# Kernel optimization log

Hardware: AMD Instinct MI355X
Metric: run time of the kernel (lower is better)

The kernel has to match this reference:

```python
import jax, jax.numpy as jnp
from jax import lax
import numpy as np

B = 4096
L = 20  # nb_latents


def conv2d(x, w, b, stride, pad):
    y = lax.conv_general_dilated(x, w, (stride, stride), [(pad, pad), (pad, pad)],
                                 dimension_numbers=('NCHW', 'OIHW', 'NCHW'))
    return y + b[None, :, None, None]


def deconv2d(x, w, b, stride, pad):
    # w has PyTorch ConvTranspose2d layout [Cin, Cout, kh, kw]
    k = w.shape[2]
    w2 = jnp.flip(w, (2, 3)).transpose(1, 0, 2, 3)  # -> [Cout, Cin, kh, kw]
    y = lax.conv_general_dilated(x, w2, (1, 1), [(k - 1 - pad,) * 2] * 2,
                                 lhs_dilation=(stride, stride),
                                 dimension_numbers=('NCHW', 'OIHW', 'NCHW'))
    return y + b[None, :, None, None]


def setup_inputs() -> dict:
    key = jax.random.key(0)
    ks = jax.random.split(key, 16)

    def W(k, shape, fan_in, scale=1.0):
        return (jax.random.normal(k, shape, jnp.float32) * (scale / np.sqrt(fan_in))).astype(jnp.float32)

    z = lambda n: jnp.zeros((n,), jnp.float32)
    return {
        'x': jax.random.uniform(ks[0], (B, 1, 28, 28), jnp.float32),
        'eps': jax.random.normal(ks[1], (B, L), jnp.float32),
        'w_c1': W(ks[2], (32, 1, 4, 4), 16), 'b_c1': z(32),
        'w_c2': W(ks[3], (32, 32, 4, 4), 512), 'b_c2': z(32),
        'w_c3': W(ks[4], (64, 32, 3, 3), 288), 'b_c3': z(64),
        'w_fc1': W(ks[5], (256, 1024), 1024), 'b_fc1': z(256),
        'w_mu': W(ks[6], (L, 256), 256), 'b_mu': z(L),
        # small scale + negative bias keeps the 100-step exp(logvar) recursion in fp32 range
        'w_ls': W(ks[7], (L, 256), 256, 0.1), 'b_ls': jnp.full((L,), -2.0, jnp.float32),
        'w_fc2': W(ks[8], (256, L), L), 'b_fc2': z(256),
        'w_fc3': W(ks[9], (1024, 256), 256), 'b_fc3': z(1024),
        'w_d1': W(ks[10], (64, 32, 3, 3), 576), 'b_d1': z(32),
        'w_d2': W(ks[11], (32, 32, 4, 4), 512), 'b_d2': z(32),
        'w_d3': W(ks[12], (32, 1, 4, 4), 512), 'b_d3': z(1),
    }


def reference(x, eps, w_c1, b_c1, w_c2, b_c2, w_c3, b_c3, w_fc1, b_fc1,
              w_mu, b_mu, w_ls, b_ls, w_fc2, b_fc2, w_fc3, b_fc3,
              w_d1, b_d1, w_d2, b_d2, w_d3, b_d3):
    # ---- encoder ----
    h = jax.nn.relu(conv2d(x, w_c1, b_c1, 2, 1))   # [B,32,14,14]
    h = jax.nn.relu(conv2d(h, w_c2, b_c2, 2, 1))   # [B,32,7,7]
    h = jax.nn.relu(conv2d(h, w_c3, b_c3, 2, 1))   # [B,64,4,4]
    h = jax.nn.relu(h.reshape(-1, 64 * 4 * 4) @ w_fc1.T + b_fc1)
    mu = h @ w_mu.T + b_mu          # [B,L]
    logvar = h @ w_ls.T + b_ls      # [B,L]

    # ---- reversing: 100 gradient-ascent steps on KLD (eval-mode reparameterize) ----
    # KLD = -0.5 * sum(1 + ls - mu^2 - exp(ls))  =>  dKLD/dmu = mu, dKLD/dls = 0.5*(exp(ls)-1)
    lr = 0.1
    def step(c, _):
        m, s = c
        return (m + lr * m, s + lr * 0.5 * (jnp.exp(s) - 1.0)), None
    (mu_r, ls_r), _ = lax.scan(step, (mu, logvar), None, length=100)
    zlat = eps * jnp.exp(0.5 * ls_r) + mu_r

    # ---- decoder ----
    d = jax.nn.relu(zlat @ w_fc2.T + b_fc2)
    d = jax.nn.relu(d @ w_fc3.T + b_fc3).reshape(-1, 64, 4, 4)
    d = jax.nn.relu(deconv2d(d, w_d1, b_d1, 2, 1))       # [B,32,7,7]
    d = jax.nn.relu(deconv2d(d, w_d2, b_d2, 2, 1))       # [B,32,14,14]
    x_hat = jax.nn.sigmoid(deconv2d(d, w_d3, b_d3, 2, 1))  # [B,1,28,28]
    return x_hat, mu, logvar
```

## Files before the change

kernel.cpp:

```cpp
#include <hip/hip_runtime.h>
#include <math.h>

#define BATCH 4096

__device__ __forceinline__ void dot4a(float& acc, const float4 v, const float4 wt) {
    acc = fmaf(v.x, wt.x, acc);
    acc = fmaf(v.y, wt.y, acc);
    acc = fmaf(v.z, wt.z, acc);
    acc = fmaf(v.w, wt.w, acc);
}

__global__ __launch_bounds__(256) void tr_kernel(
    const float* __restrict__ w_c2, const float* __restrict__ w_c3,
    const float* __restrict__ w_d1, const float* __restrict__ w_d2,
    const float* __restrict__ w_d3,
    float* __restrict__ wt2, float* __restrict__ wt3,
    float* __restrict__ wtd1, float* __restrict__ wtd2, float* __restrict__ wtd3)
{
    int i = blockIdx.x * 256 + threadIdx.x;
    if (i < 16384) {
        int ci = i & 31, tap = (i >> 5) & 15, co = i >> 9;
        wt2[i] = w_c2[(co * 32 + ci) * 16 + tap];
    }
    if (i < 18432) {
        int ci = i & 31, r = i >> 5, tap = r % 9, co = r / 9;
        wt3[i] = w_c3[(co * 32 + ci) * 9 + tap];
    }
    if (i < 18432) {
        int ci = i & 63, r = i >> 6, tap = r % 9, co = r / 9;
        wtd1[i] = w_d1[(ci * 32 + co) * 9 + tap];
    }
    if (i < 16384) {
        int ci = i & 31, tap = (i >> 5) & 15, co = i >> 9;
        wtd2[i] = w_d2[(ci * 32 + co) * 16 + tap];
    }
    if (i < 512) {
        int ci = i & 31, tap = i >> 5;
        wtd3[i] = w_d3[ci * 16 + tap];
    }
}

__global__ __launch_bounds__(256, 3) void enc_kernel(
    const float* __restrict__ x,
    const float* __restrict__ w_c1, const float* __restrict__ b_c1,
    const float* __restrict__ wt2, const float* __restrict__ b_c2,
    const float* __restrict__ wt3, const float* __restrict__ b_c3,
    float* __restrict__ h3out)
{
    __shared__ __align__(16) float buf[12708];
    float* s_h1 = buf;
    float* s_h3 = buf;
    float* s_x  = buf + 9216;
    float* s_h2 = buf + 10116;

    const int n = blockIdx.x, tid = threadIdx.x;
    const int wv = __builtin_amdgcn_readfirstlane((int)(tid >> 6));
    const int lane = tid & 63;
    const int co0 = wv * 8;

    {
        float4* z1 = (float4*)buf;
        #pragma unroll
        for (int i = tid; i < 2304; i += 256) z1[i] = make_float4(0.f, 0.f, 0.f, 0.f);
        float4* z2 = (float4*)(buf + 10116);
        for (int i = tid; i < 648; i += 256) z2[i] = make_float4(0.f, 0.f, 0.f, 0.f);
        for (int i = tid; i < 30; i += 256) { s_x[i] = 0.f; s_x[870 + i] = 0.f; }
        for (int i = tid; i < 28; i += 256) { s_x[(i + 1) * 30] = 0.f; s_x[(i + 1) * 30 + 29] = 0.f; }
        for (int i = tid; i < 784; i += 256) {
            int iy = i / 28, ix = i - iy * 28;
            s_x[(iy + 1) * 30 + ix + 1] = x[(size_t)n * 784 + i];
        }
    }
    __syncthreads();

    {
        const int poff = lane & 15, pr = lane >> 4;
        const int ca = co0 + pr * 2;
        float w1a[16], w1b[16];
        #pragma unroll
        for (int k = 0; k < 4; ++k) {
            *(float4*)&w1a[4 * k] = *(const float4*)(w_c1 + ca * 16 + 4 * k);
            *(float4*)&w1b[4 * k] = *(const float4*)(w_c1 + (ca + 1) * 16 + 4 * k);
        }
        const float ba = b_c1[ca], bb = b_c1[ca + 1];
        for (int t = 0; t < 13; ++t) {
            int pos = poff + 16 * t;
            bool val = pos < 196;
            int p = val ? pos : 0;
            int oy = p / 14, ox = p - oy * 14;
            const float* bp = s_x + (2 * oy) * 30 + 2 * ox;
            float a0 = ba, a1 = bb;
            #pragma unroll
            for (int ky = 0; ky < 4; ++ky)
                #pragma unroll
                for (int kx = 0; kx < 4; ++kx) {
                    float v = bp[ky * 30 + kx];
                    a0 = fmaf(v, w1a[ky * 4 + kx], a0);
                    a1 = fmaf(v, w1b[ky * 4 + kx], a1);
                }
            if (val)
                *(float2*)(s_h1 + ((oy + 1) * 16 + ox + 1) * 36 + ca) =
                    make_float2(fmaxf(a0, 0.f), fmaxf(a1, 0.f));
        }
    }
    __syncthreads();

    {
        const int parity = lane & 1, pr = (lane >> 1) & 3, cig = lane >> 3;
        const int ca = co0 + pr * 2;
        float4 w2a[16], w2b[16];
        #pragma unroll
        for (int t = 0; t < 16; ++t) {
            w2a[t] = *(const float4*)(wt2 + (ca * 16 + t) * 32 + cig * 4);
            w2b[t] = *(const float4*)(wt2 + ((ca + 1) * 16 + t) * 32 + cig * 4);
        }
        const float ba = b_c2[ca], bb = b_c2[ca + 1];
        for (int t = 0; t < 25; ++t) {
            int pos = parity + 2 * t;
            bool val = pos < 49;
            int p = val ? pos : 0;
            int oy = p / 7, ox = p - oy * 7;
            const float* bp = s_h1 + ((2 * oy) * 16 + 2 * ox) * 36 + cig * 4;
            float a0 = 0.f, a1 = 0.f;
            #pragma unroll
            for (int ky = 0; ky < 4; ++ky)
                #pragma unroll
                for (int kx = 0; kx < 4; ++kx) {
                    float4 v = *(const float4*)(bp + (ky * 16 + kx) * 36);
                    dot4a(a0, v, w2a[ky * 4 + kx]);
                    dot4a(a1, v, w2b[ky * 4 + kx]);
                }
            a0 += __shfl_xor(a0, 8);  a1 += __shfl_xor(a1, 8);
            a0 += __shfl_xor(a0, 16); a1 += __shfl_xor(a1, 16);
            a0 += __shfl_xor(a0, 32); a1 += __shfl_xor(a1, 32);
            if (cig == 0 && val)
                *(float2*)(s_h2 + ((oy + 1) * 9 + ox + 1) * 32 + ca) =
                    make_float2(fmaxf(a0 + ba, 0.f), fmaxf(a1 + bb, 0.f));
        }
    }
    __syncthreads();

    {
        const int pr = lane & 7, cig = lane >> 3;
        const int ca = wv * 16 + pr * 2;
        float4 w3a[9], w3b[9];
        #pragma unroll
        for (int t = 0; t < 9; ++t) {
            w3a[t] = *(const float4*)(wt3 + (ca * 9 + t) * 32 + cig * 4);
            w3b[t] = *(const float4*)(wt3 + ((ca + 1) * 9 + t) * 32 + cig * 4);
        }
        const float ba = b_c3[ca], bb = b_c3[ca + 1];
        #pragma unroll 2
        for (int pos = 0; pos < 16; ++pos) {
            int oy = pos >> 2, ox = pos & 3;
            const float* bp = s_h2 + ((2 * oy) * 9 + 2 * ox) * 32 + cig * 4;
            float a0 = 0.f, a1 = 0.f;
            #pragma unroll
            for (int ky = 0; ky < 3; ++ky)
                #pragma unroll
                for (int kx = 0; kx < 3; ++kx) {
                    float4 v = *(const float4*)(bp + (ky * 9 + kx) * 32);
                    dot4a(a0, v, w3a[ky * 3 + kx]);
                    dot4a(a1, v, w3b[ky * 3 + kx]);
                }
            a0 += __shfl_xor(a0, 8);  a1 += __shfl_xor(a1, 8);
            a0 += __shfl_xor(a0, 16); a1 += __shfl_xor(a1, 16);
            a0 += __shfl_xor(a0, 32); a1 += __shfl_xor(a1, 32);
            if (cig == 0) {
                s_h3[ca * 16 + pos] = fmaxf(a0 + ba, 0.f);
                s_h3[(ca + 1) * 16 + pos] = fmaxf(a1 + bb, 0.f);
            }
        }
    }
    __syncthreads();
    for (int i = tid; i < 1024; i += 256) h3out[(size_t)n * 1024 + i] = s_h3[i];
}

template <bool RELU>
__global__ __launch_bounds__(256) void gemm_nt(
    const float* __restrict__ A, const float* __restrict__ W,
    const float* __restrict__ bias, float* __restrict__ C,
    int M, int N, int K)
{
    __shared__ float As[16][65];
    __shared__ float Ws[16][65];
    const int tid = threadIdx.x;
    const int col0 = blockIdx.x * 64;
    const int row0 = blockIdx.y * 64;
    const int tx = tid & 15, ty = tid >> 4;
    const int lr = tid >> 2, lc = (tid & 3) * 4;
    float acc[4][4] = {};

    for (int k0 = 0; k0 < K; k0 += 16) {
        float4 av = *(const float4*)(A + (size_t)(row0 + lr) * K + k0 + lc);
        float4 wv = *(const float4*)(W + (size_t)(col0 + lr) * K + k0 + lc);
        As[lc + 0][lr] = av.x; As[lc + 1][lr] = av.y; As[lc + 2][lr] = av.z; As[lc + 3][lr] = av.w;
        Ws[lc + 0][lr] = wv.x; Ws[lc + 1][lr] = wv.y; Ws[lc + 2][lr] = wv.z; Ws[lc + 3][lr] = wv.w;
        __syncthreads();
        #pragma unroll
        for (int kk = 0; kk < 16; ++kk) {
            float a[4], b[4];
            #pragma unroll
            for (int i = 0; i < 4; ++i) a[i] = As[kk][ty * 4 + i];
            #pragma unroll
            for (int j = 0; j < 4; ++j) b[j] = Ws[kk][tx * 4 + j];
            #pragma unroll
            for (int i = 0; i < 4; ++i)
                #pragma unroll
                for (int j = 0; j < 4; ++j)
                    acc[i][j] = fmaf(a[i], b[j], acc[i][j]);
        }
        __syncthreads();
    }
    #pragma unroll
    for (int i = 0; i < 4; ++i) {
        int row = row0 + ty * 4 + i;
        float* cp = C + (size_t)row * N + col0 + tx * 4;
        float4 v;
        v.x = acc[i][0] + bias[col0 + tx * 4 + 0];
        v.y = acc[i][1] + bias[col0 + tx * 4 + 1];
        v.z = acc[i][2] + bias[col0 + tx * 4 + 2];
        v.w = acc[i][3] + bias[col0 + tx * 4 + 3];
        if (RELU) {
            v.x = fmaxf(v.x, 0.f); v.y = fmaxf(v.y, 0.f);
            v.z = fmaxf(v.z, 0.f); v.w = fmaxf(v.w, 0.f);
        }
        *(float4*)cp = v;
    }
}

__global__ __launch_bounds__(256) void mulsrev_kernel(
    const float* __restrict__ h,
    const float* __restrict__ w_mu, const float* __restrict__ b_mu,
    const float* __restrict__ w_ls, const float* __restrict__ b_ls,
    const float* __restrict__ eps,
    float* __restrict__ mu_out, float* __restrict__ ls_out, float* __restrict__ z)
{
    int idx = blockIdx.x * 256 + threadIdx.x;
    if (idx >= BATCH * 20) return;
    int i = idx / 20, j = idx - i * 20;
    const float4* hp = (const float4*)(h + (size_t)i * 256);
    const float4* mp = (const float4*)(w_mu + j * 256);
    const float4* lp = (const float4*)(w_ls + j * 256);
    float am = b_mu[j], al = b_ls[j];
    #pragma unroll 8
    for (int k = 0; k < 64; ++k) {
        float4 hv = hp[k], mv = mp[k], lv = lp[k];
        am = fmaf(hv.x, mv.x, am); al = fmaf(hv.x, lv.x, al);
        am = fmaf(hv.y, mv.y, am); al = fmaf(hv.y, lv.y, al);
        am = fmaf(hv.z, mv.z, am); al = fmaf(hv.z, lv.z, al);
        am = fmaf(hv.w, mv.w, am); al = fmaf(hv.w, lv.w, al);
    }
    mu_out[idx] = am;
    ls_out[idx] = al;
    double m = (double)am;
    float s = al;
    #pragma unroll 4
    for (int t = 0; t < 100; ++t) {
        m += 0.1 * m;
        s += 0.05f * (expf(s) - 1.f);
    }
    z[idx] = fmaf(eps[idx], expf(0.5f * s), (float)m);
}

__global__ __launch_bounds__(256) void fc2_kernel(
    const float* __restrict__ z, const float* __restrict__ w, const float* __restrict__ b,
    float* __restrict__ out)
{
    int idx = blockIdx.x * 256 + threadIdx.x;
    int i = idx >> 8, j = idx & 255;
    float acc = b[j];
    const float* zp = z + i * 20;
    const float* wp = w + j * 20;
    #pragma unroll
    for (int k = 0; k < 20; ++k) acc = fmaf(zp[k], wp[k], acc);
    out[idx] = fmaxf(acc, 0.f);
}

__global__ __launch_bounds__(256, 3) void dec_kernel(
    const float* __restrict__ hin,
    const float* __restrict__ wtd1, const float* __restrict__ b_d1,
    const float* __restrict__ wtd2, const float* __restrict__ b_d2,
    const float* __restrict__ wtd3, const float* __restrict__ b_d3,
    float* __restrict__ xhat)
{
    __shared__ __align__(16) float dbuf[11060];
    float* s_d2 = dbuf;
    float* s_d1 = dbuf + 7056;
    float* s_in = dbuf + 9972;
    float* sP   = dbuf + 7056;

    const int n = blockIdx.x, tid = threadIdx.x;
    const int wv = __builtin_amdgcn_readfirstlane((int)(tid >> 6));
    const int lane = tid & 63;
    const int co0 = wv * 8;

    {
        float4* z1 = (float4*)(dbuf + 7056);
        for (int i = tid; i < 729; i += 256) z1[i] = make_float4(0.f, 0.f, 0.f, 0.f);
        for (int t = tid; t < 1024; t += 256) {
            int c = t & 63, p = t >> 6;
            s_in[p * 68 + c] = hin[(size_t)n * 1024 + c * 16 + p];
        }
    }
    __syncthreads();

    {
        const int cig = lane & 7, pq = (lane >> 3) & 1, poff = lane >> 4;
        const int ci0 = cig * 8;
        const int ca = co0 + pq * 4;
        float bd[4];
        #pragma unroll
        for (int u = 0; u < 4; ++u) bd[u] = b_d1[ca + u];

        #pragma unroll
        for (int py = 0; py < 2; ++py) {
            #pragma unroll
            for (int px = 0; px < 2; ++px) {
                const int ny = 4 - py, nx = 4 - px;
                const int P = ny * nx;
                const int na = py ? 2 : 1, nb = px ? 2 : 1;
                float4 wd[4][2][2][2];
                #pragma unroll
                for (int u = 0; u < 4; ++u)
                    #pragma unroll
                    for (int a = 0; a < 2; ++a) {
                        if (a >= na) continue;
                        #pragma unroll
                        for (int b = 0; b < 2; ++b) {
                            if (b >= nb) continue;
                            int ky = py ? (a ? 2 : 0) : 1;
                            int kx = px ? (b ? 2 : 0) : 1;
                            const float* wp = wtd1 + ((ca + u) * 9 + ky * 3 + kx) * 64 + ci0;
                            wd[u][a][b][0] = *(const float4*)(wp);
                            wd[u][a][b][1] = *(const float4*)(wp + 4);
                        }
                    }
                const int niter = (P + 3) >> 2;
                for (int it = 0; it < niter; ++it) {
                    int pidx = it * 4 + poff;
                    bool act = pidx < P;
                    int p = act ? pidx : 0;
                    int sy = p / nx, sx = p - sy * nx;
                    float acc[4] = {};
                    #pragma unroll
                    for (int a = 0; a < 2; ++a) {
                        if (a >= na) continue;
                        int iy = py ? (a ? sy : sy + 1) : sy;
                        #pragma unroll
                        for (int b = 0; b < 2; ++b) {
                            if (b >= nb) continue;
                            int ix = px ? (b ? sx : sx + 1) : sx;
                            const float* bp = s_in + (iy * 4 + ix) * 68 + ci0;
                            float4 v0 = *(const float4*)(bp);
                            float4 v1 = *(const float4*)(bp + 4);
                            #pragma unroll
                            for (int u = 0; u < 4; ++u) {
                                dot4a(acc[u], v0, wd[u][a][b][0]);
                                dot4a(acc[u], v1, wd[u][a][b][1]);
                            }
                        }
                    }
                    #pragma unroll
                    for (int u = 0; u < 4; ++u) {
                        acc[u] += __shfl_xor(acc[u], 1);
                        acc[u] += __shfl_xor(acc[u], 2);
                        acc[u] += __shfl_xor(acc[u], 4);
                    }
                    if (cig == 0 && act) {
                        int oy = 2 * sy + py, ox = 2 * sx + px;
                        float4 o;
                        o.x = fmaxf(acc[0] + bd[0], 0.f);
                        o.y = fmaxf(acc[1] + bd[1], 0.f);
                        o.z = fmaxf(acc[2] + bd[2], 0.f);
                        o.w = fmaxf(acc[3] + bd[3], 0.f);
                        *(float4*)(s_d1 + ((oy + 1) * 9 + ox + 1) * 36 + ca) = o;
                    }
                }
            }
        }
    }
    __syncthreads();

    {
        const int cig = lane & 3, pq = (lane >> 2) & 1;
        const int py = (lane >> 3) & 1, px = (lane >> 4) & 1, poff = lane >> 5;
        const int ci0 = cig * 8;
        const int ca = co0 + pq * 4;
        float4 w2[4][2][2][2];
        float bd[4];
        #pragma unroll
        for (int u = 0; u < 4; ++u) {
            bd[u] = b_d2[ca + u];
            #pragma unroll
            for (int a = 0; a < 2; ++a)
                #pragma unroll
                for (int b = 0; b < 2; ++b) {
                    int ky = py ? (a ? 2 : 0) : (a ? 3 : 1);
                    int kx = px ? (b ? 2 : 0) : (b ? 3 : 1);
                    const float* wp = wtd2 + ((ca + u) * 16 + ky * 4 + kx) * 32 + ci0;
                    w2[u][a][b][0] = *(const float4*)(wp);
                    w2[u][a][b][1] = *(const float4*)(wp + 4);
                }
        }
        for (int it = 0; it < 25; ++it) {
            int pidx = it * 2 + poff;
            bool act = pidx < 49;
            int sp = act ? pidx : 0;
            int sy = sp / 7, sx = sp - sy * 7;
            float acc[4] = {};
            #pragma unroll
            for (int a = 0; a < 2; ++a) {
                int iy = py ? (a ? sy : sy + 1) : (a ? sy - 1 : sy);
                #pragma unroll
                for (int b = 0; b < 2; ++b) {
                    int ix = px ? (b ? sx : sx + 1) : (b ? sx - 1 : sx);
                    const float* bp = s_d1 + ((iy + 1) * 9 + ix + 1) * 36 + ci0;
                    float4 v0 = *(const float4*)(bp);
                    float4 v1 = *(const float4*)(bp + 4);
                    #pragma unroll
                    for (int u = 0; u < 4; ++u) {
                        dot4a(acc[u], v0, w2[u][a][b][0]);
                        dot4a(acc[u], v1, w2[u][a][b][1]);
                    }
                }
            }
            #pragma unroll
            for (int u = 0; u < 4; ++u) {
                acc[u] += __shfl_xor(acc[u], 1);
                acc[u] += __shfl_xor(acc[u], 2);
            }
            if (cig == 0 && act) {
                int oy = 2 * sy + py, ox = 2 * sx + px;
                float4 o;
                o.x = fmaxf(acc[0] + bd[0], 0.f);
                o.y = fmaxf(acc[1] + bd[1], 0.f);
                o.z = fmaxf(acc[2] + bd[2], 0.f);
                o.w = fmaxf(acc[3] + bd[3], 0.f);
                *(float4*)(s_d2 + (oy * 14 + ox) * 36 + ca) = o;
            }
        }
    }
    __syncthreads();

    {
        const int pp = lane & 15, tq = lane >> 4;
        float4 w3[4][8];
        #pragma unroll
        for (int j = 0; j < 4; ++j)
            #pragma unroll
            for (int q = 0; q < 8; ++q)
                w3[j][q] = *(const float4*)(wtd3 + (tq * 4 + j) * 32 + q * 4);
        #pragma unroll
        for (int r = 0; r < 4; ++r) {
            int p = r * 64 + wv * 16 + pp;
            if (p < 196) {
                const float* bp = s_d2 + p * 36;
                float4 v[8];
                #pragma unroll
                for (int q = 0; q < 8; ++q) v[q] = *(const float4*)(bp + q * 4);
                #pragma unroll
                for (int j = 0; j < 4; ++j) {
                    float acc = 0.f;
                    #pragma unroll
                    for (int q = 0; q < 8; ++q) dot4a(acc, v[q], w3[j][q]);
                    sP[(tq * 4 + j) * 196 + p] = acc;
                }
            }
        }
    }
    __syncthreads();

    {
        const float bd3 = b_d3[0];
        #pragma unroll
        for (int t = 0; t < 4; ++t) {
            int o = t * 256 + tid;
            if (o < 784) {
                int oy = o / 28, ox = o - oy * 28;
                int py = oy & 1, px = ox & 1, sy = oy >> 1, sx = ox >> 1;
                float acc = bd3;
                #pragma unroll
                for (int a = 0; a < 2; ++a) {
                    int ky = py ? (a ? 2 : 0) : (a ? 3 : 1);
                    int iy = py ? (a ? sy : sy + 1) : (a ? sy - 1 : sy);
                    bool vy = (unsigned)iy < 14u;
                    #pragma unroll
                    for (int b = 0; b < 2; ++b) {
                        int kx = px ? (b ? 2 : 0) : (b ? 3 : 1);
                        int ix = px ? (b ? sx : sx + 1) : (b ? sx - 1 : sx);
                        if (vy && (unsigned)ix < 14u)
                            acc += sP[(ky * 4 + kx) * 196 + iy * 14 + ix];
                    }
                }
                xhat[(size_t)n * 784 + o] = 1.f / (1.f + expf(-acc));
            }
        }
    }
}

extern "C" void kernel_launch(void* const* d_in, const int* in_sizes, int n_in,
                              void* d_out, int out_size, void* d_ws, size_t ws_size,
                              hipStream_t stream) {
    const float* x     = (const float*)d_in[0];
    const float* eps   = (const float*)d_in[1];
    const float* w_c1  = (const float*)d_in[2];
    const float* b_c1  = (const float*)d_in[3];
    const float* w_c2  = (const float*)d_in[4];
    const float* b_c2  = (const float*)d_in[5];
    const float* w_c3  = (const float*)d_in[6];
    const float* b_c3  = (const float*)d_in[7];
    const float* w_fc1 = (const float*)d_in[8];
    const float* b_fc1 = (const float*)d_in[9];
    const float* w_mu  = (const float*)d_in[10];
    const float* b_mu  = (const float*)d_in[11];
    const float* w_ls  = (const float*)d_in[12];
    const float* b_ls  = (const float*)d_in[13];
    const float* w_fc2 = (const float*)d_in[14];
    const float* b_fc2 = (const float*)d_in[15];
    const float* w_fc3 = (const float*)d_in[16];
    const float* b_fc3 = (const float*)d_in[17];
    const float* w_d1  = (const float*)d_in[18];
    const float* b_d1  = (const float*)d_in[19];
    const float* w_d2  = (const float*)d_in[20];
    const float* b_d2  = (const float*)d_in[21];
    const float* w_d3  = (const float*)d_in[22];
    const float* b_d3  = (const float*)d_in[23];

    float* out = (float*)d_out;
    float* x_hat  = out;
    float* mu_out = out + 4096 * 784;
    float* ls_out = mu_out + 4096 * 20;

    float* buf1 = (float*)d_ws;
    float* buf2 = buf1 + 4096 * 1024;
    float* zlat = buf1;
    float* wt2  = buf2 + 4096 * 256;
    float* wt3  = wt2 + 16384;
    float* wtd1 = wt3 + 18432;
    float* wtd2 = wtd1 + 18432;
    float* wtd3 = wtd2 + 16384;

    tr_kernel<<<72, 256, 0, stream>>>(w_c2, w_c3, w_d1, w_d2, w_d3, wt2, wt3, wtd1, wtd2, wtd3);
    enc_kernel<<<BATCH, 256, 0, stream>>>(x, w_c1, b_c1, wt2, b_c2, wt3, b_c3, buf1);
    gemm_nt<true><<<dim3(256 / 64, BATCH / 64), 256, 0, stream>>>(buf1, w_fc1, b_fc1, buf2, BATCH, 256, 1024);
    mulsrev_kernel<<<(BATCH * 20) / 256, 256, 0, stream>>>(buf2, w_mu, b_mu, w_ls, b_ls, eps, mu_out, ls_out, zlat);
    fc2_kernel<<<BATCH, 256, 0, stream>>>(zlat, w_fc2, b_fc2, buf2);
    gemm_nt<true><<<dim3(1024 / 64, BATCH / 64), 256, 0, stream>>>(buf2, w_fc3, b_fc3, buf1, BATCH, 1024, 256);
    dec_kernel<<<BATCH, 256, 0, stream>>>(buf1, wtd1, b_d1, wtd2, b_d2, wtd3, b_d3, x_hat);
}
```

Baseline: 648.8 us.

## Shrink shared-memory footprint to raise occupancy and retile fc GEMMs

Encoder and decoder kernels drop padded rows and channel padding from their shared-memory activation layouts. Out-of-range row reads are clamped to a single zeroed row, which lets the LDS buffers shrink and the launch bound rise from 3 to 4 blocks per CU. The fully connected GEMM moves to 512 threads with a 32-deep K tile and 2x4 outputs per thread. Risks are LDS bank conflicts from the unpadded stride of 32 and lower per-thread reuse in the GEMM.

```diff
diff --git a/kernel.cpp b/kernel.cpp
--- a/kernel.cpp
+++ b/kernel.cpp
@@ -40,18 +40,18 @@
     }
 }
 
-__global__ __launch_bounds__(256, 3) void enc_kernel(
+__global__ __launch_bounds__(256, 4) void enc_kernel(
     const float* __restrict__ x,
     const float* __restrict__ w_c1, const float* __restrict__ b_c1,
     const float* __restrict__ wt2, const float* __restrict__ b_c2,
     const float* __restrict__ wt3, const float* __restrict__ b_c3,
     float* __restrict__ h3out)
 {
-    __shared__ __align__(16) float buf[12708];
+    __shared__ __align__(16) float buf[9984];
     float* s_h1 = buf;
     float* s_h3 = buf;
-    float* s_x  = buf + 9216;
-    float* s_h2 = buf + 10116;
+    float* s_x  = buf + 7680;
+    float* s_h2 = buf + 7680;
 
     const int n = blockIdx.x, tid = threadIdx.x;
     const int wv = __builtin_amdgcn_readfirstlane((int)(tid >> 6));
@@ -61,9 +61,7 @@
     {
         float4* z1 = (float4*)buf;
         #pragma unroll
-        for (int i = tid; i < 2304; i += 256) z1[i] = make_float4(0.f, 0.f, 0.f, 0.f);
-        float4* z2 = (float4*)(buf + 10116);
-        for (int i = tid; i < 648; i += 256) z2[i] = make_float4(0.f, 0.f, 0.f, 0.f);
+        for (int i = tid; i < 1920; i += 256) z1[i] = make_float4(0.f, 0.f, 0.f, 0.f);
         for (int i = tid; i < 30; i += 256) { s_x[i] = 0.f; s_x[870 + i] = 0.f; }
         for (int i = tid; i < 28; i += 256) { s_x[(i + 1) * 30] = 0.f; s_x[(i + 1) * 30 + 29] = 0.f; }
         for (int i = tid; i < 784; i += 256) {
@@ -99,11 +97,22 @@
                     a1 = fmaf(v, w1b[ky * 4 + kx], a1);
                 }
             if (val)
-                *(float2*)(s_h1 + ((oy + 1) * 16 + ox + 1) * 36 + ca) =
+                *(float2*)(s_h1 + (oy * 16 + ox + 1) * 32 + ca) =
                     make_float2(fmaxf(a0, 0.f), fmaxf(a1, 0.f));
         }
     }
     __syncthreads();
+
+    {
+        float4* h2v = (float4*)s_h2;
+        for (int i = tid; i < 184; i += 256) {
+            int off;
+            if (i < 72) off = 504 + i;
+            else if (i < 128) { int j = i - 72; off = (j >> 3) * 72 + (j & 7); }
+            else { int j = i - 128; off = (j >> 3) * 72 + 64 + (j & 7); }
+            h2v[off] = make_float4(0.f, 0.f, 0.f, 0.f);
+        }
+    }
 
     {
         const int parity = lane & 1, pr = (lane >> 1) & 3, cig = lane >> 3;
@@ -120,21 +129,24 @@
             bool val = pos < 49;
             int p = val ? pos : 0;
             int oy = p / 7, ox = p - oy * 7;
-            const float* bp = s_h1 + ((2 * oy) * 16 + 2 * ox) * 36 + cig * 4;
             float a0 = 0.f, a1 = 0.f;
             #pragma unroll
-            for (int ky = 0; ky < 4; ++ky)
+            for (int ky = 0; ky < 4; ++ky) {
+                int iy = 2 * oy - 1 + ky;
+                int row = ((unsigned)iy < 14u) ? iy : 14;
+                const float* bp = s_h1 + row * 512 + (2 * ox) * 32 + cig * 4;
                 #pragma unroll
                 for (int kx = 0; kx < 4; ++kx) {
-                    float4 v = *(const float4*)(bp + (ky * 16 + kx) * 36);
+                    float4 v = *(const float4*)(bp + kx * 32);
                     dot4a(a0, v, w2a[ky * 4 + kx]);
                     dot4a(a1, v, w2b[ky * 4 + kx]);
                 }
+            }
             a0 += __shfl_xor(a0, 8);  a1 += __shfl_xor(a1, 8);
             a0 += __shfl_xor(a0, 16); a1 += __shfl_xor(a1, 16);
             a0 += __shfl_xor(a0, 32); a1 += __shfl_xor(a1, 32);
             if (cig == 0 && val)
-                *(float2*)(s_h2 + ((oy + 1) * 9 + ox + 1) * 32 + ca) =
+                *(float2*)(s_h2 + (oy * 9 + ox + 1) * 32 + ca) =
                     make_float2(fmaxf(a0 + ba, 0.f), fmaxf(a1 + bb, 0.f));
         }
     }
@@ -153,16 +165,19 @@
         #pragma unroll 2
         for (int pos = 0; pos < 16; ++pos) {
             int oy = pos >> 2, ox = pos & 3;
-            const float* bp = s_h2 + ((2 * oy) * 9 + 2 * ox) * 32 + cig * 4;
             float a0 = 0.f, a1 = 0.f;
             #pragma unroll
-            for (int ky = 0; ky < 3; ++ky)
+            for (int ky = 0; ky < 3; ++ky) {
+                int iy = 2 * oy - 1 + ky;
+                int row = ((unsigned)iy < 7u) ? iy : 7;
+                const float* bp = s_h2 + row * 288 + (2 * ox) * 32 + cig * 4;
                 #pragma unroll
                 for (int kx = 0; kx < 3; ++kx) {
-                    float4 v = *(const float4*)(bp + (ky * 9 + kx) * 32);
+                    float4 v = *(const float4*)(bp + kx * 32);
                     dot4a(a0, v, w3a[ky * 3 + kx]);
                     dot4a(a1, v, w3b[ky * 3 + kx]);
                 }
+            }
             a0 += __shfl_xor(a0, 8);  a1 += __shfl_xor(a1, 8);
             a0 += __shfl_xor(a0, 16); a1 += __shfl_xor(a1, 16);
             a0 += __shfl_xor(a0, 32); a1 += __shfl_xor(a1, 32);
@@ -177,44 +192,43 @@
 }
 
 template <bool RELU>
-__global__ __launch_bounds__(256) void gemm_nt(
+__global__ __launch_bounds__(512) void gemm_nt(
     const float* __restrict__ A, const float* __restrict__ W,
     const float* __restrict__ bias, float* __restrict__ C,
     int M, int N, int K)
 {
-    __shared__ float As[16][65];
-    __shared__ float Ws[16][65];
+    __shared__ float As[32][65];
+    __shared__ float Ws[32][65];
     const int tid = threadIdx.x;
     const int col0 = blockIdx.x * 64;
     const int row0 = blockIdx.y * 64;
     const int tx = tid & 15, ty = tid >> 4;
-    const int lr = tid >> 2, lc = (tid & 3) * 4;
-    float acc[4][4] = {};
-
-    for (int k0 = 0; k0 < K; k0 += 16) {
+    const int lr = tid >> 3, lc = (tid & 7) * 4;
+    float acc[2][4] = {};
+
+    for (int k0 = 0; k0 < K; k0 += 32) {
         float4 av = *(const float4*)(A + (size_t)(row0 + lr) * K + k0 + lc);
         float4 wv = *(const float4*)(W + (size_t)(col0 + lr) * K + k0 + lc);
         As[lc + 0][lr] = av.x; As[lc + 1][lr] = av.y; As[lc + 2][lr] = av.z; As[lc + 3][lr] = av.w;
         Ws[lc + 0][lr] = wv.x; Ws[lc + 1][lr] = wv.y; Ws[lc + 2][lr] = wv.z; Ws[lc + 3][lr] = wv.w;
         __syncthreads();
         #pragma unroll
-        for (int kk = 0; kk < 16; ++kk) {
-            float a[4], b[4];
-            #pragma unroll
-            for (int i = 0; i < 4; ++i) a[i] = As[kk][ty * 4 + i];
+        for (int kk = 0; kk < 32; ++kk) {
+            float a0 = As[kk][ty * 2], a1 = As[kk][ty * 2 + 1];
+            float b[4];
             #pragma unroll
             for (int j = 0; j < 4; ++j) b[j] = Ws[kk][tx * 4 + j];
             #pragma unroll
-            for (int i = 0; i < 4; ++i)
-                #pragma unroll
-                for (int j = 0; j < 4; ++j)
-                    acc[i][j] = fmaf(a[i], b[j], acc[i][j]);
+            for (int j = 0; j < 4; ++j) {
+                acc[0][j] = fmaf(a0, b[j], acc[0][j]);
+                acc[1][j] = fmaf(a1, b[j], acc[1][j]);
+            }
         }
         __syncthreads();
     }
     #pragma unroll
-    for (int i = 0; i < 4; ++i) {
-        int row = row0 + ty * 4 + i;
+    for (int i = 0; i < 2; ++i) {
+        int row = row0 + ty * 2 + i;
         float* cp = C + (size_t)row * N + col0 + tx * 4;
         float4 v;
         v.x = acc[i][0] + bias[col0 + tx * 4 + 0];
@@ -277,18 +291,18 @@
     out[idx] = fmaxf(acc, 0.f);
 }
 
-__global__ __launch_bounds__(256, 3) void dec_kernel(
+__global__ __launch_bounds__(256, 4) void dec_kernel(
     const float* __restrict__ hin,
     const float* __restrict__ wtd1, const float* __restrict__ b_d1,
     const float* __restrict__ wtd2, const float* __restrict__ b_d2,
     const float* __restrict__ wtd3, const float* __restrict__ b_d3,
     float* __restrict__ xhat)
 {
-    __shared__ __align__(16) float dbuf[11060];
+    __shared__ __align__(16) float dbuf[9952];
     float* s_d2 = dbuf;
-    float* s_d1 = dbuf + 7056;
-    float* s_in = dbuf + 9972;
-    float* sP   = dbuf + 7056;
+    float* s_d1 = dbuf + 6272;
+    float* s_in = dbuf + 8864;
+    float* sP   = dbuf + 6272;
 
     const int n = blockIdx.x, tid = threadIdx.x;
     const int wv = __builtin_amdgcn_readfirstlane((int)(tid >> 6));
@@ -296,8 +310,8 @@
     const int co0 = wv * 8;
 
     {
-        float4* z1 = (float4*)(dbuf + 7056);
-        for (int i = tid; i < 729; i += 256) z1[i] = make_float4(0.f, 0.f, 0.f, 0.f);
+        float4* z1 = (float4*)s_d1;
+        for (int i = tid; i < 648; i += 256) z1[i] = make_float4(0.f, 0.f, 0.f, 0.f);
         for (int t = tid; t < 1024; t += 256) {
             int c = t & 63, p = t >> 6;
             s_in[p * 68 + c] = hin[(size_t)n * 1024 + c * 16 + p];
@@ -374,7 +388,7 @@
                         o.y = fmaxf(acc[1] + bd[1], 0.f);
                         o.z = fmaxf(acc[2] + bd[2], 0.f);
                         o.w = fmaxf(acc[3] + bd[3], 0.f);
-                        *(float4*)(s_d1 + ((oy + 1) * 9 + ox + 1) * 36 + ca) = o;
+                        *(float4*)(s_d1 + (oy * 9 + ox + 1) * 36 + ca) = o;
                     }
                 }
             }
@@ -412,10 +426,11 @@
             #pragma unroll
             for (int a = 0; a < 2; ++a) {
                 int iy = py ? (a ? sy : sy + 1) : (a ? sy - 1 : sy);
+                int row = ((unsigned)iy < 7u) ? iy : 7;
                 #pragma unroll
                 for (int b = 0; b < 2; ++b) {
                     int ix = px ? (b ? sx : sx + 1) : (b ? sx - 1 : sx);
-                    const float* bp = s_d1 + ((iy + 1) * 9 + ix + 1) * 36 + ci0;
+                    const float* bp = s_d1 + (row * 9 + ix + 1) * 36 + ci0;
                     float4 v0 = *(const float4*)(bp);
                     float4 v1 = *(const float4*)(bp + 4);
                     #pragma unroll
@@ -437,7 +452,7 @@
                 o.y = fmaxf(acc[1] + bd[1], 0.f);
                 o.z = fmaxf(acc[2] + bd[2], 0.f);
                 o.w = fmaxf(acc[3] + bd[3], 0.f);
-                *(float4*)(s_d2 + (oy * 14 + ox) * 36 + ca) = o;
+                *(float4*)(s_d2 + (oy * 14 + ox) * 32 + ca) = o;
             }
         }
     }
@@ -455,7 +470,7 @@
         for (int r = 0; r < 4; ++r) {
             int p = r * 64 + wv * 16 + pp;
             if (p < 196) {
-                const float* bp = s_d2 + p * 36;
+                const float* bp = s_d2 + p * 32;
                 float4 v[8];
                 #pragma unroll
                 for (int q = 0; q < 8; ++q) v[q] = *(const float4*)(bp + q * 4);
@@ -543,9 +558,9 @@
 
     tr_kernel<<<72, 256, 0, stream>>>(w_c2, w_c3, w_d1, w_d2, w_d3, wt2, wt3, wtd1, wtd2, wtd3);
     enc_kernel<<<BATCH, 256, 0, stream>>>(x, w_c1, b_c1, wt2, b_c2, wt3, b_c3, buf1);
-    gemm_nt<true><<<dim3(256 / 64, BATCH / 64), 256, 0, stream>>>(buf1, w_fc1, b_fc1, buf2, BATCH, 256, 1024);
+    gemm_nt<true><<<dim3(256 / 64, BATCH / 64), 512, 0, stream>>>(buf1, w_fc1, b_fc1, buf2, BATCH, 256, 1024);
     mulsrev_kernel<<<(BATCH * 20) / 256, 256, 0, stream>>>(buf2, w_mu, b_mu, w_ls, b_ls, eps, mu_out, ls_out, zlat);
     fc2_kernel<<<BATCH, 256, 0, stream>>>(zlat, w_fc2, b_fc2, buf2);
-    gemm_nt<true><<<dim3(1024 / 64, BATCH / 64), 256, 0, stream>>>(buf2, w_fc3, b_fc3, buf1, BATCH, 1024, 256);
+    gemm_nt<true><<<dim3(1024 / 64, BATCH / 64), 512, 0, stream>>>(buf2, w_fc3, b_fc3, buf1, BATCH, 1024, 256);
     dec_kernel<<<BATCH, 256, 0, stream>>>(buf1, wtd1, b_d1, wtd2, b_d2, wtd3, b_d3, x_hat);
 }
```

After: 1.403 ms. +116.3%, slower.
